# Performance work log

Hardware: AMD Instinct MI355X
Metric: run time of the kernel (lower is better)

The kernel has to match this reference:

```python
import jax, jax.numpy as jnp
import numpy as np

ALPHA = 0.2  # LeakyReLU negative slope
NEG_INF = -9e15


def setup_inputs() -> dict:
    key = jax.random.key(0)
    k1, k2, k3, k4 = jax.random.split(key, 4)
    N, F_in, F_out = 8192, 256, 64
    h = jax.random.normal(k1, (N, F_in), dtype=jnp.float32)
    adj = jax.random.randint(k2, (N, N), 0, 2, dtype=jnp.int32)
    # xavier-uniform-style scaling for params
    W = jax.random.normal(k3, (F_in, F_out), dtype=jnp.float32) * (1.0 / np.sqrt(F_in))
    a = jax.random.normal(k4, (2 * F_out, 1), dtype=jnp.float32) * (1.0 / np.sqrt(F_out))
    return {"h": h, "adj": adj, "W": W, "a": a}


def reference(h, adj, W, a):
    # Wh: [N, F_out]
    Wh = h @ W
    F_out = W.shape[1]
    a1 = a[:F_out, 0]   # attends to source (row i)
    a2 = a[F_out:, 0]   # attends to target (row j)
    f1 = Wh @ a1        # [N]
    f2 = Wh @ a2        # [N]
    # e[i, j] = leakyrelu(Wh_i . a1 + Wh_j . a2)  == original repeat/cat math
    e = jax.nn.leaky_relu(f1[:, None] + f2[None, :], negative_slope=ALPHA)
    attention = jnp.where(adj > 0, e, NEG_INF)
    attention = jax.nn.softmax(attention, axis=1)
    # dropout omitted (eval / deterministic reference)
    h_prime = attention @ Wh  # [N, F_out]
    return jax.nn.elu(h_prime)
```

## Files before the change

### kernel.cpp

```cpp
#include <hip/hip_runtime.h>
#include <hip/hip_bf16.h>
#include <stdint.h>

#define N 8192
#define FIN 256
#define FOUT 64
#define WAVES 8
#define JLEN (N / WAVES)

typedef __attribute__((ext_vector_type(8))) short s8v;
typedef __attribute__((ext_vector_type(4))) float f4v;

__device__ __forceinline__ uint32_t f2bf(float f) {
  uint32_t u = __float_as_uint(f);
  return (u + 0x7FFFu + ((u >> 16) & 1u)) >> 16;
}

__global__ __launch_bounds__(256) void gat_prep(
    const float* __restrict__ h, const float* __restrict__ W,
    const float* __restrict__ a,
    float* __restrict__ f1, float* __restrict__ f2,
    uint16_t* __restrict__ whT)
{
  const int c = threadIdx.x & 63;
  const int wave = threadIdx.x >> 6;
  const int i0 = blockIdx.x * 16 + wave * 4;
  float acc[4] = {0.f, 0.f, 0.f, 0.f};
  #pragma unroll 8
  for (int k = 0; k < FIN; ++k) {
    float wv = W[k * FOUT + c];
    #pragma unroll
    for (int r = 0; r < 4; ++r)
      acc[r] += h[(size_t)(i0 + r) * FIN + k] * wv;
  }
  uint32_t b0 = f2bf(acc[0]), b1 = f2bf(acc[1]), b2 = f2bf(acc[2]), b3 = f2bf(acc[3]);
  int2 pk;
  pk.x = (int)(b0 | (b1 << 16));
  pk.y = (int)(b2 | (b3 << 16));
  *(int2*)(whT + (size_t)c * N + i0) = pk;

  const float a1 = a[c], a2 = a[FOUT + c];
  const float LOG2E = 1.4426950408889634f;
  #pragma unroll
  for (int r = 0; r < 4; ++r) {
    float v1 = acc[r] * a1;
    float v2 = acc[r] * a2;
    #pragma unroll
    for (int m = 32; m > 0; m >>= 1) {
      v1 += __shfl_xor(v1, m, 64);
      v2 += __shfl_xor(v2, m, 64);
    }
    if (c == 0) { f1[i0 + r] = v1 * LOG2E; f2[i0 + r] = v2 * LOG2E; }
  }
}

__device__ __forceinline__ s8v make_afrag(float f1v, int4 c0, int4 c1,
                                          float4 g0, float4 g1, float& den) {
  float e0 = f1v + g0.x; e0 = fmaxf(e0, 0.2f * e0); float w0 = (c0.x > 0) ? __builtin_exp2f(e0) : 0.f;
  float e1 = f1v + g0.y; e1 = fmaxf(e1, 0.2f * e1); float w1 = (c0.y > 0) ? __builtin_exp2f(e1) : 0.f;
  float e2 = f1v + g0.z; e2 = fmaxf(e2, 0.2f * e2); float w2 = (c0.z > 0) ? __builtin_exp2f(e2) : 0.f;
  float e3 = f1v + g0.w; e3 = fmaxf(e3, 0.2f * e3); float w3 = (c0.w > 0) ? __builtin_exp2f(e3) : 0.f;
  float e4 = f1v + g1.x; e4 = fmaxf(e4, 0.2f * e4); float w4 = (c1.x > 0) ? __builtin_exp2f(e4) : 0.f;
  float e5 = f1v + g1.y; e5 = fmaxf(e5, 0.2f * e5); float w5 = (c1.y > 0) ? __builtin_exp2f(e5) : 0.f;
  float e6 = f1v + g1.z; e6 = fmaxf(e6, 0.2f * e6); float w6 = (c1.z > 0) ? __builtin_exp2f(e6) : 0.f;
  float e7 = f1v + g1.w; e7 = fmaxf(e7, 0.2f * e7); float w7 = (c1.w > 0) ? __builtin_exp2f(e7) : 0.f;
  uint32_t b0 = f2bf(w0), b1 = f2bf(w1), b2 = f2bf(w2), b3 = f2bf(w3);
  uint32_t b4 = f2bf(w4), b5 = f2bf(w5), b6 = f2bf(w6), b7 = f2bf(w7);
  den += __uint_as_float(b0 << 16) + __uint_as_float(b1 << 16)
       + __uint_as_float(b2 << 16) + __uint_as_float(b3 << 16)
       + __uint_as_float(b4 << 16) + __uint_as_float(b5 << 16)
       + __uint_as_float(b6 << 16) + __uint_as_float(b7 << 16);
  union { s8v v; uint32_t u[4]; } r;
  r.u[0] = b0 | (b1 << 16);
  r.u[1] = b2 | (b3 << 16);
  r.u[2] = b4 | (b5 << 16);
  r.u[3] = b6 | (b7 << 16);
  return r.v;
}

__global__ __launch_bounds__(512, 4) void gat_fused(
    const int* __restrict__ adj, const float* __restrict__ f1,
    const float* __restrict__ f2, const uint16_t* __restrict__ whT,
    float* __restrict__ out)
{
  __shared__ __align__(16) float lds_f2[WAVES][JLEN];
  __shared__ __align__(16) float lds_num[WAVES][16][64];
  __shared__ float lds_den[WAVES][16];

  const int t = threadIdx.x;
  const int w = t >> 6;
  const int lane = t & 63;
  const int i0 = blockIdx.x * 16;
  const int jb = w * JLEN;
  const int m  = lane & 15;
  const int kg = lane >> 4;

  const float f1v = f1[i0 + m];
  const int*      ap  = adj + (size_t)(i0 + m) * N + jb + kg * 8;
  const uint16_t* bp0 = whT + (size_t)m * N + jb + kg * 8;

  int4 A0 = *(const int4*)(ap);
  int4 A1 = *(const int4*)(ap + 4);
  int4 A2 = *(const int4*)(ap + 32);
  int4 A3 = *(const int4*)(ap + 36);

  #pragma unroll
  for (int q = 0; q < 4; ++q)
    *(float4*)&lds_f2[w][q * 256 + lane * 4] =
        *(const float4*)&f2[jb + q * 256 + lane * 4];

  const float4* lf = (const float4*)&lds_f2[w][0];
  const int kg2 = kg * 2;

  f4v acc0 = {0.f, 0.f, 0.f, 0.f};
  f4v acc1 = acc0, acc2 = acc0, acc3 = acc0;
  float den = 0.f;

  int4 B0, B1, B2, B3;

#define COMPUTE(C0, C1, C2, C3, J) do {                                     \
    const uint16_t* bp = bp0 + (J);                                         \
    s8v b00 = *(const s8v*)(bp);                                            \
    s8v b01 = *(const s8v*)(bp + 32);                                       \
    s8v b10 = *(const s8v*)(bp + 16 * N);                                   \
    s8v b11 = *(const s8v*)(bp + 16 * N + 32);                              \
    s8v b20 = *(const s8v*)(bp + 32 * N);                                   \
    s8v b21 = *(const s8v*)(bp + 32 * N + 32);                              \
    s8v b30 = *(const s8v*)(bp + 48 * N);                                   \
    s8v b31 = *(const s8v*)(bp + 48 * N + 32);                              \
    float4 g0 = lf[((J) >> 2) + kg2];                                       \
    float4 g1 = lf[((J) >> 2) + kg2 + 1];                                   \
    float4 g2 = lf[((J) >> 2) + kg2 + 8];                                   \
    float4 g3 = lf[((J) >> 2) + kg2 + 9];                                   \
    s8v a0 = make_afrag(f1v, C0, C1, g0, g1, den);                          \
    s8v a1 = make_afrag(f1v, C2, C3, g2, g3, den);                          \
    acc0 = __builtin_amdgcn_mfma_f32_16x16x32_bf16(a0, b00, acc0, 0, 0, 0); \
    acc0 = __builtin_amdgcn_mfma_f32_16x16x32_bf16(a1, b01, acc0, 0, 0, 0); \
    acc1 = __builtin_amdgcn_mfma_f32_16x16x32_bf16(a0, b10, acc1, 0, 0, 0); \
    acc1 = __builtin_amdgcn_mfma_f32_16x16x32_bf16(a1, b11, acc1, 0, 0, 0); \
    acc2 = __builtin_amdgcn_mfma_f32_16x16x32_bf16(a0, b20, acc2, 0, 0, 0); \
    acc2 = __builtin_amdgcn_mfma_f32_16x16x32_bf16(a1, b21, acc2, 0, 0, 0); \
    acc3 = __builtin_amdgcn_mfma_f32_16x16x32_bf16(a0, b30, acc3, 0, 0, 0); \
    acc3 = __builtin_amdgcn_mfma_f32_16x16x32_bf16(a1, b31, acc3, 0, 0, 0); \
  } while (0)

  #pragma unroll 1
  for (int jc2 = 0; jc2 < 8; ++jc2) {
    const int j0 = jc2 * 128;
    B0 = *(const int4*)(ap + j0 + 64);
    B1 = *(const int4*)(ap + j0 + 68);
    B2 = *(const int4*)(ap + j0 + 96);
    B3 = *(const int4*)(ap + j0 + 100);
    COMPUTE(A0, A1, A2, A3, j0);
    if (jc2 < 7) {
      A0 = *(const int4*)(ap + j0 + 128);
      A1 = *(const int4*)(ap + j0 + 132);
      A2 = *(const int4*)(ap + j0 + 160);
      A3 = *(const int4*)(ap + j0 + 164);
    }
    COMPUTE(B0, B1, B2, B3, j0 + 64);
  }
#undef COMPUTE

  den += __shfl_xor(den, 16, 64);
  den += __shfl_xor(den, 32, 64);

  float* np = &lds_num[w][0][0];
  #pragma unroll
  for (int r = 0; r < 4; ++r) {
    int row = kg * 4 + r;
    np[row * 64 +      m] = acc0[r];
    np[row * 64 + 16 + m] = acc1[r];
    np[row * 64 + 32 + m] = acc2[r];
    np[row * 64 + 48 + m] = acc3[r];
  }
  if (lane < 16) lds_den[w][m] = den;
  __syncthreads();

  const int col = t & 63;
  const int r0 = t >> 6;
  #pragma unroll
  for (int hh = 0; hh < 2; ++hh) {
    const int row = r0 + hh * 8;
    float num = 0.f, dsum = 0.f;
    #pragma unroll
    for (int q = 0; q < WAVES; ++q) {
      num  += lds_num[q][row][col];
      dsum += lds_den[q][row];
    }
    float hp = num / dsum;
    out[(size_t)(i0 + row) * 64 + col] = (hp > 0.f) ? hp : (__expf(hp) - 1.f);
  }
}

extern "C" void kernel_launch(void* const* d_in, const int* in_sizes, int n_in,
                              void* d_out, int out_size, void* d_ws, size_t ws_size,
                              hipStream_t stream) {
  const float* h   = (const float*)d_in[0];
  const int*   adj = (const int*)d_in[1];
  const float* W   = (const float*)d_in[2];
  const float* a   = (const float*)d_in[3];
  float* out = (float*)d_out;

  float* f1 = (float*)d_ws;
  float* f2 = f1 + N;
  uint16_t* whT = (uint16_t*)(f2 + N);

  gat_prep<<<N / 16, 256, 0, stream>>>(h, W, a, f1, f2, whT);
  gat_fused<<<N / 16, 512, 0, stream>>>(adj, f1, f2, whT, out);
}
```

Baseline: 431.0 us.

## Pack adjacency into bitmask in prep kernel and consume bits in fused kernel

The prep kernel gains extra blocks that read the int32 adjacency matrix once and compress it with wave ballots into a 1-bit-per-entry mask in workspace. The fused attention kernel then reads this mask instead of the full int32 adjacency. It applies the mask with bitwise AND on the exp results rather than compares and selects. The f2 staging through LDS is dropped in favour of direct global loads. The full 256 MB adjacency read is still paid once in prep, so the gain depends on the fused kernel's adjacency traffic and any overlap of the bitmask pass with the Wh projection.

```diff
diff --git a/kernel.cpp b/kernel.cpp
--- a/kernel.cpp
+++ b/kernel.cpp
@@ -7,6 +7,9 @@
 #define FOUT 64
 #define WAVES 8
 #define JLEN (N / WAVES)
+#define PREP_BLOCKS 256
+#define CMP_BLOCKS 768
+#define NGROUP ((N * N) / 512)
 
 typedef __attribute__((ext_vector_type(8))) short s8v;
 typedef __attribute__((ext_vector_type(4))) float f4v;
@@ -16,15 +19,42 @@
   return (u + 0x7FFFu + ((u >> 16) & 1u)) >> 16;
 }
 
-__global__ __launch_bounds__(256) void gat_prep(
+__global__ __launch_bounds__(512) void gat_pre(
     const float* __restrict__ h, const float* __restrict__ W,
-    const float* __restrict__ a,
+    const float* __restrict__ a, const int* __restrict__ adj,
     float* __restrict__ f1, float* __restrict__ f2,
-    uint16_t* __restrict__ whT)
+    uint16_t* __restrict__ whT, unsigned long long* __restrict__ bm)
 {
-  const int c = threadIdx.x & 63;
+  const int lane = threadIdx.x & 63;
   const int wave = threadIdx.x >> 6;
-  const int i0 = blockIdx.x * 16 + wave * 4;
+
+  if (blockIdx.x >= PREP_BLOCKS) {
+    const int wv = ((blockIdx.x - PREP_BLOCKS) << 3) + wave;
+    const int NW = CMP_BLOCKS * 8;
+    for (int g = wv; g < NGROUP; g += NW) {
+      const int* p = adj + (size_t)g * 512 + lane;
+      unsigned long long b0 = __ballot(p[0]   > 0);
+      unsigned long long b1 = __ballot(p[64]  > 0);
+      unsigned long long b2 = __ballot(p[128] > 0);
+      unsigned long long b3 = __ballot(p[192] > 0);
+      unsigned long long b4 = __ballot(p[256] > 0);
+      unsigned long long b5 = __ballot(p[320] > 0);
+      unsigned long long b6 = __ballot(p[384] > 0);
+      unsigned long long b7 = __ballot(p[448] > 0);
+      if (lane == 0) {
+        ulonglong2* q = (ulonglong2*)(bm + (size_t)g * 8);
+        ulonglong2 v;
+        v.x = b0; v.y = b1; q[0] = v;
+        v.x = b2; v.y = b3; q[1] = v;
+        v.x = b4; v.y = b5; q[2] = v;
+        v.x = b6; v.y = b7; q[3] = v;
+      }
+    }
+    return;
+  }
+
+  const int c = lane;
+  const int i0 = blockIdx.x * 32 + wave * 4;
   float acc[4] = {0.f, 0.f, 0.f, 0.f};
   #pragma unroll 8
   for (int k = 0; k < FIN; ++k) {
@@ -54,16 +84,18 @@
   }
 }
 
-__device__ __forceinline__ s8v make_afrag(float f1v, int4 c0, int4 c1,
+#define MASKW(w, b) __uint_as_float(__float_as_uint(w) & \
+                    (uint32_t)(((int)(ub << (31 - (b)))) >> 31))
+__device__ __forceinline__ s8v make_afrag(float f1v, uint32_t ub,
                                           float4 g0, float4 g1, float& den) {
-  float e0 = f1v + g0.x; e0 = fmaxf(e0, 0.2f * e0); float w0 = (c0.x > 0) ? __builtin_exp2f(e0) : 0.f;
-  float e1 = f1v + g0.y; e1 = fmaxf(e1, 0.2f * e1); float w1 = (c0.y > 0) ? __builtin_exp2f(e1) : 0.f;
-  float e2 = f1v + g0.z; e2 = fmaxf(e2, 0.2f * e2); float w2 = (c0.z > 0) ? __builtin_exp2f(e2) : 0.f;
-  float e3 = f1v + g0.w; e3 = fmaxf(e3, 0.2f * e3); float w3 = (c0.w > 0) ? __builtin_exp2f(e3) : 0.f;
-  float e4 = f1v + g1.x; e4 = fmaxf(e4, 0.2f * e4); float w4 = (c1.x > 0) ? __builtin_exp2f(e4) : 0.f;
-  float e5 = f1v + g1.y; e5 = fmaxf(e5, 0.2f * e5); float w5 = (c1.y > 0) ? __builtin_exp2f(e5) : 0.f;
-  float e6 = f1v + g1.z; e6 = fmaxf(e6, 0.2f * e6); float w6 = (c1.z > 0) ? __builtin_exp2f(e6) : 0.f;
-  float e7 = f1v + g1.w; e7 = fmaxf(e7, 0.2f * e7); float w7 = (c1.w > 0) ? __builtin_exp2f(e7) : 0.f;
+  float e0 = f1v + g0.x; e0 = fmaxf(e0, 0.2f * e0); float w0 = MASKW(__builtin_exp2f(e0), 0);
+  float e1 = f1v + g0.y; e1 = fmaxf(e1, 0.2f * e1); float w1 = MASKW(__builtin_exp2f(e1), 1);
+  float e2 = f1v + g0.z; e2 = fmaxf(e2, 0.2f * e2); float w2 = MASKW(__builtin_exp2f(e2), 2);
+  float e3 = f1v + g0.w; e3 = fmaxf(e3, 0.2f * e3); float w3 = MASKW(__builtin_exp2f(e3), 3);
+  float e4 = f1v + g1.x; e4 = fmaxf(e4, 0.2f * e4); float w4 = MASKW(__builtin_exp2f(e4), 4);
+  float e5 = f1v + g1.y; e5 = fmaxf(e5, 0.2f * e5); float w5 = MASKW(__builtin_exp2f(e5), 5);
+  float e6 = f1v + g1.z; e6 = fmaxf(e6, 0.2f * e6); float w6 = MASKW(__builtin_exp2f(e6), 6);
+  float e7 = f1v + g1.w; e7 = fmaxf(e7, 0.2f * e7); float w7 = MASKW(__builtin_exp2f(e7), 7);
   uint32_t b0 = f2bf(w0), b1 = f2bf(w1), b2 = f2bf(w2), b3 = f2bf(w3);
   uint32_t b4 = f2bf(w4), b5 = f2bf(w5), b6 = f2bf(w6), b7 = f2bf(w7);
   den += __uint_as_float(b0 << 16) + __uint_as_float(b1 << 16)
@@ -79,11 +111,10 @@
 }
 
 __global__ __launch_bounds__(512, 4) void gat_fused(
-    const int* __restrict__ adj, const float* __restrict__ f1,
+    const uint32_t* __restrict__ bm, const float* __restrict__ f1,
     const float* __restrict__ f2, const uint16_t* __restrict__ whT,
     float* __restrict__ out)
 {
-  __shared__ __align__(16) float lds_f2[WAVES][JLEN];
   __shared__ __align__(16) float lds_num[WAVES][16][64];
   __shared__ float lds_den[WAVES][16];
 
@@ -94,73 +125,48 @@
   const int jb = w * JLEN;
   const int m  = lane & 15;
   const int kg = lane >> 4;
+  const int kg8 = kg * 8;
 
   const float f1v = f1[i0 + m];
-  const int*      ap  = adj + (size_t)(i0 + m) * N + jb + kg * 8;
-  const uint16_t* bp0 = whT + (size_t)m * N + jb + kg * 8;
-
-  int4 A0 = *(const int4*)(ap);
-  int4 A1 = *(const int4*)(ap + 4);
-  int4 A2 = *(const int4*)(ap + 32);
-  int4 A3 = *(const int4*)(ap + 36);
-
-  #pragma unroll
-  for (int q = 0; q < 4; ++q)
-    *(float4*)&lds_f2[w][q * 256 + lane * 4] =
-        *(const float4*)&f2[jb + q * 256 + lane * 4];
-
-  const float4* lf = (const float4*)&lds_f2[w][0];
-  const int kg2 = kg * 2;
+  const uint32_t* bmr = bm + (size_t)(i0 + m) * (N / 32) + (jb >> 5);
+  const uint16_t* bp0 = whT + (size_t)m * N + jb + kg8;
+  const float*    fpb = f2 + jb + kg8;
 
   f4v acc0 = {0.f, 0.f, 0.f, 0.f};
   f4v acc1 = acc0, acc2 = acc0, acc3 = acc0;
   float den = 0.f;
 
-  int4 B0, B1, B2, B3;
-
-#define COMPUTE(C0, C1, C2, C3, J) do {                                     \
-    const uint16_t* bp = bp0 + (J);                                         \
-    s8v b00 = *(const s8v*)(bp);                                            \
-    s8v b01 = *(const s8v*)(bp + 32);                                       \
-    s8v b10 = *(const s8v*)(bp + 16 * N);                                   \
-    s8v b11 = *(const s8v*)(bp + 16 * N + 32);                              \
-    s8v b20 = *(const s8v*)(bp + 32 * N);                                   \
-    s8v b21 = *(const s8v*)(bp + 32 * N + 32);                              \
-    s8v b30 = *(const s8v*)(bp + 48 * N);                                   \
-    s8v b31 = *(const s8v*)(bp + 48 * N + 32);                              \
-    float4 g0 = lf[((J) >> 2) + kg2];                                       \
-    float4 g1 = lf[((J) >> 2) + kg2 + 1];                                   \
-    float4 g2 = lf[((J) >> 2) + kg2 + 8];                                   \
-    float4 g3 = lf[((J) >> 2) + kg2 + 9];                                   \
-    s8v a0 = make_afrag(f1v, C0, C1, g0, g1, den);                          \
-    s8v a1 = make_afrag(f1v, C2, C3, g2, g3, den);                          \
-    acc0 = __builtin_amdgcn_mfma_f32_16x16x32_bf16(a0, b00, acc0, 0, 0, 0); \
-    acc0 = __builtin_amdgcn_mfma_f32_16x16x32_bf16(a1, b01, acc0, 0, 0, 0); \
-    acc1 = __builtin_amdgcn_mfma_f32_16x16x32_bf16(a0, b10, acc1, 0, 0, 0); \
-    acc1 = __builtin_amdgcn_mfma_f32_16x16x32_bf16(a1, b11, acc1, 0, 0, 0); \
-    acc2 = __builtin_amdgcn_mfma_f32_16x16x32_bf16(a0, b20, acc2, 0, 0, 0); \
-    acc2 = __builtin_amdgcn_mfma_f32_16x16x32_bf16(a1, b21, acc2, 0, 0, 0); \
-    acc3 = __builtin_amdgcn_mfma_f32_16x16x32_bf16(a0, b30, acc3, 0, 0, 0); \
-    acc3 = __builtin_amdgcn_mfma_f32_16x16x32_bf16(a1, b31, acc3, 0, 0, 0); \
-  } while (0)
-
-  #pragma unroll 1
-  for (int jc2 = 0; jc2 < 8; ++jc2) {
-    const int j0 = jc2 * 128;
-    B0 = *(const int4*)(ap + j0 + 64);
-    B1 = *(const int4*)(ap + j0 + 68);
-    B2 = *(const int4*)(ap + j0 + 96);
-    B3 = *(const int4*)(ap + j0 + 100);
-    COMPUTE(A0, A1, A2, A3, j0);
-    if (jc2 < 7) {
-      A0 = *(const int4*)(ap + j0 + 128);
-      A1 = *(const int4*)(ap + j0 + 132);
-      A2 = *(const int4*)(ap + j0 + 160);
-      A3 = *(const int4*)(ap + j0 + 164);
-    }
-    COMPUTE(B0, B1, B2, B3, j0 + 64);
-  }
-#undef COMPUTE
+  #pragma unroll 2
+  for (int jc = 0; jc < 16; ++jc) {
+    const int j0 = jc * 64;
+    uint2 bits = *(const uint2*)(bmr + (j0 >> 5));
+    uint32_t ub0 = (bits.x >> kg8) & 0xffu;
+    uint32_t ub1 = (bits.y >> kg8) & 0xffu;
+    const float* fp = fpb + j0;
+    float4 g0 = *(const float4*)(fp);
+    float4 g1 = *(const float4*)(fp + 4);
+    float4 g2 = *(const float4*)(fp + 32);
+    float4 g3 = *(const float4*)(fp + 36);
+    const uint16_t* bp = bp0 + j0;
+    s8v b00 = *(const s8v*)(bp);
+    s8v b01 = *(const s8v*)(bp + 32);
+    s8v b10 = *(const s8v*)(bp + 16 * N);
+    s8v b11 = *(const s8v*)(bp + 16 * N + 32);
+    s8v b20 = *(const s8v*)(bp + 32 * N);
+    s8v b21 = *(const s8v*)(bp + 32 * N + 32);
+    s8v b30 = *(const s8v*)(bp + 48 * N);
+    s8v b31 = *(const s8v*)(bp + 48 * N + 32);
+    s8v a0 = make_afrag(f1v, ub0, g0, g1, den);
+    s8v a1 = make_afrag(f1v, ub1, g2, g3, den);
+    acc0 = __builtin_amdgcn_mfma_f32_16x16x32_bf16(a0, b00, acc0, 0, 0, 0);
+    acc0 = __builtin_amdgcn_mfma_f32_16x16x32_bf16(a1, b01, acc0, 0, 0, 0);
+    acc1 = __builtin_amdgcn_mfma_f32_16x16x32_bf16(a0, b10, acc1, 0, 0, 0);
+    acc1 = __builtin_amdgcn_mfma_f32_16x16x32_bf16(a1, b11, acc1, 0, 0, 0);
+    acc2 = __builtin_amdgcn_mfma_f32_16x16x32_bf16(a0, b20, acc2, 0, 0, 0);
+    acc2 = __builtin_amdgcn_mfma_f32_16x16x32_bf16(a1, b21, acc2, 0, 0, 0);
+    acc3 = __builtin_amdgcn_mfma_f32_16x16x32_bf16(a0, b30, acc3, 0, 0, 0);
+    acc3 = __builtin_amdgcn_mfma_f32_16x16x32_bf16(a1, b31, acc3, 0, 0, 0);
+  }
 
   den += __shfl_xor(den, 16, 64);
   den += __shfl_xor(den, 32, 64);
@@ -205,7 +211,9 @@
   float* f1 = (float*)d_ws;
   float* f2 = f1 + N;
   uint16_t* whT = (uint16_t*)(f2 + N);
-
-  gat_prep<<<N / 16, 256, 0, stream>>>(h, W, a, f1, f2, whT);
-  gat_fused<<<N / 16, 512, 0, stream>>>(adj, f1, f2, whT, out);
-}
+  unsigned long long* bm = (unsigned long long*)(whT + (size_t)FOUT * N);
+
+  gat_pre<<<PREP_BLOCKS + CMP_BLOCKS, 512, 0, stream>>>(h, W, a, adj,
+                                                        f1, f2, whT, bm);
+  gat_fused<<<N / 16, 512, 0, stream>>>((const uint32_t*)bm, f1, f2, whT, out);
+}
```

New measurement: 450.6 us. 1.05x slower.

## Compute softmax denominator with MFMA, use packed bf16 convert, load f2 directly

Applied to the files above, without the earlier changes.

The softmax denominator is now accumulated by an extra pair of MFMAs against an all-ones bf16 vector, replacing the per-lane scalar sum of bf16-rounded weights and the cross-lane shuffles. The eight scalar bf16 rounding sequences are replaced with the hardware packed v_cvt_pk_bf16_f32 instruction. The per-wave LDS staging of f2 is removed in favour of direct global vector loads inside the loop. This trims VALU work in the exp/pack path, which is likely the bottleneck, at the cost of 25% more MFMA issue and more global load traffic for f2.

```diff
diff --git a/kernel.cpp b/kernel.cpp
--- a/kernel.cpp
+++ b/kernel.cpp
@@ -14,6 +14,12 @@
 __device__ __forceinline__ uint32_t f2bf(float f) {
   uint32_t u = __float_as_uint(f);
   return (u + 0x7FFFu + ((u >> 16) & 1u)) >> 16;
+}
+
+__device__ __forceinline__ uint32_t cvtpk_bf16(float lo, float hi) {
+  uint32_t r;
+  asm("v_cvt_pk_bf16_f32 %0, %1, %2" : "=v"(r) : "v"(lo), "v"(hi));
+  return r;
 }
 
 __global__ __launch_bounds__(256) void gat_prep(
@@ -55,26 +61,24 @@
 }
 
 __device__ __forceinline__ s8v make_afrag(float f1v, int4 c0, int4 c1,
-                                          float4 g0, float4 g1, float& den) {
-  float e0 = f1v + g0.x; e0 = fmaxf(e0, 0.2f * e0); float w0 = (c0.x > 0) ? __builtin_exp2f(e0) : 0.f;
-  float e1 = f1v + g0.y; e1 = fmaxf(e1, 0.2f * e1); float w1 = (c0.y > 0) ? __builtin_exp2f(e1) : 0.f;
-  float e2 = f1v + g0.z; e2 = fmaxf(e2, 0.2f * e2); float w2 = (c0.z > 0) ? __builtin_exp2f(e2) : 0.f;
-  float e3 = f1v + g0.w; e3 = fmaxf(e3, 0.2f * e3); float w3 = (c0.w > 0) ? __builtin_exp2f(e3) : 0.f;
-  float e4 = f1v + g1.x; e4 = fmaxf(e4, 0.2f * e4); float w4 = (c1.x > 0) ? __builtin_exp2f(e4) : 0.f;
-  float e5 = f1v + g1.y; e5 = fmaxf(e5, 0.2f * e5); float w5 = (c1.y > 0) ? __builtin_exp2f(e5) : 0.f;
-  float e6 = f1v + g1.z; e6 = fmaxf(e6, 0.2f * e6); float w6 = (c1.z > 0) ? __builtin_exp2f(e6) : 0.f;
-  float e7 = f1v + g1.w; e7 = fmaxf(e7, 0.2f * e7); float w7 = (c1.w > 0) ? __builtin_exp2f(e7) : 0.f;
-  uint32_t b0 = f2bf(w0), b1 = f2bf(w1), b2 = f2bf(w2), b3 = f2bf(w3);
-  uint32_t b4 = f2bf(w4), b5 = f2bf(w5), b6 = f2bf(w6), b7 = f2bf(w7);
-  den += __uint_as_float(b0 << 16) + __uint_as_float(b1 << 16)
-       + __uint_as_float(b2 << 16) + __uint_as_float(b3 << 16)
-       + __uint_as_float(b4 << 16) + __uint_as_float(b5 << 16)
-       + __uint_as_float(b6 << 16) + __uint_as_float(b7 << 16);
+                                          f4v g0, f4v g1) {
+  f4v e0 = g0 + f1v;
+  f4v e1 = g1 + f1v;
+  f4v s0 = e0 * 0.2f;
+  f4v s1 = e1 * 0.2f;
+  float w0 = __builtin_exp2f(fmaxf(e0[0], s0[0])); if (c0.x <= 0) w0 = 0.f;
+  float w1 = __builtin_exp2f(fmaxf(e0[1], s0[1])); if (c0.y <= 0) w1 = 0.f;
+  float w2 = __builtin_exp2f(fmaxf(e0[2], s0[2])); if (c0.z <= 0) w2 = 0.f;
+  float w3 = __builtin_exp2f(fmaxf(e0[3], s0[3])); if (c0.w <= 0) w3 = 0.f;
+  float w4 = __builtin_exp2f(fmaxf(e1[0], s1[0])); if (c1.x <= 0) w4 = 0.f;
+  float w5 = __builtin_exp2f(fmaxf(e1[1], s1[1])); if (c1.y <= 0) w5 = 0.f;
+  float w6 = __builtin_exp2f(fmaxf(e1[2], s1[2])); if (c1.z <= 0) w6 = 0.f;
+  float w7 = __builtin_exp2f(fmaxf(e1[3], s1[3])); if (c1.w <= 0) w7 = 0.f;
   union { s8v v; uint32_t u[4]; } r;
-  r.u[0] = b0 | (b1 << 16);
-  r.u[1] = b2 | (b3 << 16);
-  r.u[2] = b4 | (b5 << 16);
-  r.u[3] = b6 | (b7 << 16);
+  r.u[0] = cvtpk_bf16(w0, w1);
+  r.u[1] = cvtpk_bf16(w2, w3);
+  r.u[2] = cvtpk_bf16(w4, w5);
+  r.u[3] = cvtpk_bf16(w6, w7);
   return r.v;
 }
 
@@ -83,7 +87,6 @@
     const float* __restrict__ f2, const uint16_t* __restrict__ whT,
     float* __restrict__ out)
 {
-  __shared__ __align__(16) float lds_f2[WAVES][JLEN];
   __shared__ __align__(16) float lds_num[WAVES][16][64];
   __shared__ float lds_den[WAVES][16];
 
@@ -94,31 +97,33 @@
   const int jb = w * JLEN;
   const int m  = lane & 15;
   const int kg = lane >> 4;
+  const int kg8 = kg * 8;
 
   const float f1v = f1[i0 + m];
-  const int*      ap  = adj + (size_t)(i0 + m) * N + jb + kg * 8;
-  const uint16_t* bp0 = whT + (size_t)m * N + jb + kg * 8;
+  const int*      ap  = adj + (size_t)(i0 + m) * N + jb + kg8;
+  const uint16_t* bp0 = whT + (size_t)m * N + jb + kg8;
+  const float*    fpb = f2 + jb + kg8;
+
+  f4v acc0 = {0.f, 0.f, 0.f, 0.f};
+  f4v acc1 = acc0, acc2 = acc0, acc3 = acc0, accd = acc0;
+
+  union { s8v v; uint32_t u[4]; } onesu;
+  onesu.u[0] = 0x3F803F80u; onesu.u[1] = 0x3F803F80u;
+  onesu.u[2] = 0x3F803F80u; onesu.u[3] = 0x3F803F80u;
+  const s8v ones = onesu.v;
 
   int4 A0 = *(const int4*)(ap);
   int4 A1 = *(const int4*)(ap + 4);
   int4 A2 = *(const int4*)(ap + 32);
   int4 A3 = *(const int4*)(ap + 36);
-
-  #pragma unroll
-  for (int q = 0; q < 4; ++q)
-    *(float4*)&lds_f2[w][q * 256 + lane * 4] =
-        *(const float4*)&f2[jb + q * 256 + lane * 4];
-
-  const float4* lf = (const float4*)&lds_f2[w][0];
-  const int kg2 = kg * 2;
-
-  f4v acc0 = {0.f, 0.f, 0.f, 0.f};
-  f4v acc1 = acc0, acc2 = acc0, acc3 = acc0;
-  float den = 0.f;
-
   int4 B0, B1, B2, B3;
 
 #define COMPUTE(C0, C1, C2, C3, J) do {                                     \
+    const float* fp = fpb + (J);                                            \
+    f4v g0 = *(const f4v*)(fp);                                             \
+    f4v g1 = *(const f4v*)(fp + 4);                                         \
+    f4v g2 = *(const f4v*)(fp + 32);                                        \
+    f4v g3 = *(const f4v*)(fp + 36);                                        \
     const uint16_t* bp = bp0 + (J);                                         \
     s8v b00 = *(const s8v*)(bp);                                            \
     s8v b01 = *(const s8v*)(bp + 32);                                       \
@@ -128,12 +133,8 @@
     s8v b21 = *(const s8v*)(bp + 32 * N + 32);                              \
     s8v b30 = *(const s8v*)(bp + 48 * N);                                   \
     s8v b31 = *(const s8v*)(bp + 48 * N + 32);                              \
-    float4 g0 = lf[((J) >> 2) + kg2];                                       \
-    float4 g1 = lf[((J) >> 2) + kg2 + 1];                                   \
-    float4 g2 = lf[((J) >> 2) + kg2 + 8];                                   \
-    float4 g3 = lf[((J) >> 2) + kg2 + 9];                                   \
-    s8v a0 = make_afrag(f1v, C0, C1, g0, g1, den);                          \
-    s8v a1 = make_afrag(f1v, C2, C3, g2, g3, den);                          \
+    s8v a0 = make_afrag(f1v, C0, C1, g0, g1);                               \
+    s8v a1 = make_afrag(f1v, C2, C3, g2, g3);                               \
     acc0 = __builtin_amdgcn_mfma_f32_16x16x32_bf16(a0, b00, acc0, 0, 0, 0); \
     acc0 = __builtin_amdgcn_mfma_f32_16x16x32_bf16(a1, b01, acc0, 0, 0, 0); \
     acc1 = __builtin_amdgcn_mfma_f32_16x16x32_bf16(a0, b10, acc1, 0, 0, 0); \
@@ -142,6 +143,8 @@
     acc2 = __builtin_amdgcn_mfma_f32_16x16x32_bf16(a1, b21, acc2, 0, 0, 0); \
     acc3 = __builtin_amdgcn_mfma_f32_16x16x32_bf16(a0, b30, acc3, 0, 0, 0); \
     acc3 = __builtin_amdgcn_mfma_f32_16x16x32_bf16(a1, b31, acc3, 0, 0, 0); \
+    accd = __builtin_amdgcn_mfma_f32_16x16x32_bf16(a0, ones, accd, 0, 0, 0);\
+    accd = __builtin_amdgcn_mfma_f32_16x16x32_bf16(a1, ones, accd, 0, 0, 0);\
   } while (0)
 
   #pragma unroll 1
@@ -162,9 +165,6 @@
   }
 #undef COMPUTE
 
-  den += __shfl_xor(den, 16, 64);
-  den += __shfl_xor(den, 32, 64);
-
   float* np = &lds_num[w][0][0];
   #pragma unroll
   for (int r = 0; r < 4; ++r) {
@@ -174,7 +174,10 @@
     np[row * 64 + 32 + m] = acc2[r];
     np[row * 64 + 48 + m] = acc3[r];
   }
-  if (lane < 16) lds_den[w][m] = den;
+  if (m == 0) {
+    #pragma unroll
+    for (int r = 0; r < 4; ++r) lds_den[w][kg * 4 + r] = accd[r];
+  }
   __syncthreads();
 
   const int col = t & 63;
```

Measured after the change: 438.8 us. About the same (+1.8%).
